# Kernel tuning notes

Measured on AMD Instinct MI355X. Metric: run time of the kernel, lower is better.

The kernel has to match this reference:

```python
import jax, jax.numpy as jnp
import numpy as np

B, T, D, N = 16, 512, 1024, 16


def setup_inputs() -> dict:
    key = jax.random.key(0)
    ks = jax.random.split(key, 6)
    x = jax.random.normal(ks[0], (B, T, D), dtype=jnp.float32)
    h_tape_init = jax.random.normal(ks[1], (B, N, D), dtype=jnp.float32) * 0.1
    h_work_init = jnp.zeros((B, D), dtype=jnp.float32)
    W_h = jax.random.normal(ks[2], (D, D), dtype=jnp.float32) * 0.02
    W_xz = jax.random.normal(ks[3], (2 * D, D), dtype=jnp.float32) * 0.02
    b_h = jnp.zeros((D,), dtype=jnp.float32)
    W_write = jax.random.normal(ks[4], (D, D), dtype=jnp.float32) * 0.02
    return {"x": x, "h_tape_init": h_tape_init, "h_work_init": h_work_init,
            "W_h": W_h, "W_xz": W_xz, "b_h": b_h, "W_write": W_write}


def _e29a_scan(x, h_tape_init, h_work_init, W_h, W_xz, b_h, W_write):
    d = W_h.shape[0]
    scale = 1.0 / (d ** 0.5)
    xz = jnp.einsum('btd,ed->bte', x, W_xz)          # [B,T,2D]
    x_proj = xz[:, :, :d]                             # [B,T,D]
    z = xz[:, :, d:]                                  # [B,T,D]

    def step(carry, inp):
        h_tape, h_work = carry                        # [B,N,D], [B,D]
        x_proj_t, z_t = inp                           # [B,D], [B,D]
        read_scores = jnp.einsum('bd,bnd->bn', h_work, h_tape) * scale
        read_attn = jax.nn.softmax(read_scores, axis=-1)
        read_val = jnp.einsum('bn,bnd->bd', read_attn, h_tape)
        h_work_new = jnp.tanh(x_proj_t + h_work @ W_h.T + read_val + b_h)
        write_val = h_work_new @ W_write.T            # [B,D]
        write_scores = jnp.einsum('bd,bnd->bn', write_val, h_tape) * scale
        write_attn = jax.nn.softmax(write_scores, axis=-1)
        wa = write_attn[:, :, None]                   # [B,N,1]
        h_tape_new = h_tape * (1.0 - wa) + write_val[:, None, :] * wa
        gate = jax.nn.silu(z_t + read_val + h_work_new)
        output = h_work_new * gate
        return (h_tape_new, h_work_new), output

    inputs = (jnp.swapaxes(x_proj, 0, 1), jnp.swapaxes(z, 0, 1))  # [T,B,D]
    (h_tape_final, _), out_t = jax.lax.scan(step, (h_tape_init, h_work_init), inputs)
    output_all = jnp.swapaxes(out_t, 0, 1)            # [B,T,D]
    return output_all, h_tape_final


def reference(x, h_tape_init, h_work_init, W_h, W_xz, b_h, W_write):
    return _e29a_scan(x, h_tape_init, h_work_init, W_h, W_xz, b_h, W_write)
```

## Files before the change

kernel.cpp:

```cpp
#include <hip/hip_runtime.h>

typedef _Float16 half8 __attribute__((ext_vector_type(8)));
typedef _Float16 half4_t __attribute__((ext_vector_type(4)));
typedef _Float16 half2_t __attribute__((ext_vector_type(2)));
typedef float f32x4 __attribute__((ext_vector_type(4)));
typedef float f32x2 __attribute__((ext_vector_type(2)));
typedef unsigned long long u64;
typedef unsigned int u32;

#define SCALE 0.03125f

#define XZ_OFF   0ULL
#define RING_OFF 33554432ULL
#define XBF_OFF  33554432ULL
#define WXZ_OFF  50331648ULL
#define WH_OFF   54525952ULL
#define WW_OFF   56623104ULL
#define VOTE_OFF 58720256ULL
#define SEN_OFF  58724352ULL

#define SLOTB 36864ULL
#define R_WVP 0
#define R_H   32768

union Pk2 { u64 u[2]; half8 h8; };
union PkW { u32 u; half2_t h; };

__device__ __forceinline__ u64 ldq(const u64* p, bool mall) {
    return mall ? __hip_atomic_load(p, __ATOMIC_RELAXED, __HIP_MEMORY_SCOPE_AGENT) : *p;
}
__device__ __forceinline__ void stq(u64* p, u64 v, bool mall) {
    if (mall) __hip_atomic_store(p, v, __ATOMIC_RELAXED, __HIP_MEMORY_SCOPE_AGENT); else *p = v;
}
__device__ __forceinline__ u32 ldw(const u32* p, bool mall) {
    return mall ? __hip_atomic_load(p, __ATOMIC_RELAXED, __HIP_MEMORY_SCOPE_AGENT) : *p;
}
__device__ __forceinline__ void stw(u32* p, u32 v, bool mall) {
    if (mall) __hip_atomic_store(p, v, __ATOMIC_RELAXED, __HIP_MEMORY_SCOPE_AGENT); else *p = v;
}
__device__ __forceinline__ u32 ldsen(u32* p) {
    return __hip_atomic_load(p, __ATOMIC_RELAXED, __HIP_MEMORY_SCOPE_AGENT);
}
__device__ __forceinline__ void stsen(u32* p, u32 v) {
    __hip_atomic_store(p, v, __ATOMIC_RELAXED, __HIP_MEMORY_SCOPE_AGENT);
}

#define FDOT(a,b,acc) acc = __builtin_amdgcn_fdot2((a),(b),(acc),false)
__device__ __forceinline__ half2_t hp2(half8 v, int i) {
    half2_t r; r[0] = v[2*i]; r[1] = v[2*i+1]; return r;
}

__global__ void cvt_kernel(const float* __restrict__ in, _Float16* __restrict__ o, int n4) {
    int i = blockIdx.x * 256 + threadIdx.x;
    if (i < n4) {
        f32x4 v = ((const f32x4*)in)[i];
        half4_t h;
        h[0] = (_Float16)v[0]; h[1] = (_Float16)v[1];
        h[2] = (_Float16)v[2]; h[3] = (_Float16)v[3];
        ((half4_t*)o)[i] = h;
    }
}

__launch_bounds__(256, 1)
__global__ void gemm_xz(const _Float16* __restrict__ A,
                        const _Float16* __restrict__ Bw,
                        _Float16* __restrict__ C) {
    __shared__ _Float16 As[128 * 40];
    __shared__ _Float16 Bs[128 * 40];
    const int tid = threadIdx.x;
    const int m0 = blockIdx.y * 128, n0 = blockIdx.x * 128;
    const int w = tid >> 6, lane = tid & 63;
    const int mw = (w >> 1) * 64, nw = (w & 1) * 64;
    const int row = lane & 15, q = lane >> 4;
    f32x4 acc[4][4];
    #pragma unroll
    for (int mt = 0; mt < 4; mt++)
        #pragma unroll
        for (int nt = 0; nt < 4; nt++)
            acc[mt][nt] = (f32x4){0.f, 0.f, 0.f, 0.f};

    for (int k0 = 0; k0 < 1024; k0 += 32) {
        __syncthreads();
        for (int cc = tid; cc < 512; cc += 256) {
            int r = cc >> 2, kc = (cc & 3) * 8;
            *(half8*)(&As[r * 40 + kc]) = *(const half8*)(&A[(size_t)(m0 + r) * 1024 + k0 + kc]);
            *(half8*)(&Bs[r * 40 + kc]) = *(const half8*)(&Bw[(size_t)(n0 + r) * 1024 + k0 + kc]);
        }
        __syncthreads();
        half8 af[4], bf[4];
        #pragma unroll
        for (int mt = 0; mt < 4; mt++) af[mt] = *(const half8*)(&As[(mw + mt * 16 + row) * 40 + q * 8]);
        #pragma unroll
        for (int nt = 0; nt < 4; nt++) bf[nt] = *(const half8*)(&Bs[(nw + nt * 16 + row) * 40 + q * 8]);
        #pragma unroll
        for (int mt = 0; mt < 4; mt++)
            #pragma unroll
            for (int nt = 0; nt < 4; nt++)
                acc[mt][nt] = __builtin_amdgcn_mfma_f32_16x16x32_f16(af[mt], bf[nt], acc[mt][nt], 0, 0, 0);
    }
    #pragma unroll
    for (int mt = 0; mt < 4; mt++)
        #pragma unroll
        for (int nt = 0; nt < 4; nt++)
            #pragma unroll
            for (int r = 0; r < 4; r++) {
                int gm = m0 + mw + mt * 16 + q * 4 + r;
                int gn = n0 + nw + nt * 16 + row;
                C[(size_t)gm * 2048 + gn] = (_Float16)acc[mt][nt][r];
            }
}

__launch_bounds__(512, 2)
__global__ void scan_kernel(const _Float16* __restrict__ xz,
                            const float* __restrict__ tape_in,
                            const float* __restrict__ h_in,
                            const float* __restrict__ bh,
                            const _Float16* __restrict__ wh,
                            const _Float16* __restrict__ ww,
                            char* ring,
                            u32* sen,
                            u32* vote,
                            float* __restrict__ out) {
    const int bx = blockIdx.x;
    const int g = (bx & 7) * 2 + ((bx >> 3) & 1);
    const int s = bx >> 4;
    const int tid = threadIdx.x;
    const int lane = tid & 63;
    const int cc = tid >> 3, q = tid & 7;
    const int nn = tid >> 5, c32 = tid & 31;

    __shared__ __align__(16) _Float16 h_prev[1024];
    __shared__ __align__(16) _Float16 h_own[64];
    __shared__ __align__(16) float rv_l[1024];
    __shared__ float p_l[512 * 17];
    __shared__ float sc_l[16];
    __shared__ float pad_l[10000];
    __shared__ int sh_same;

    { volatile float* vp = pad_l; vp[tid] = 0.f; }

    if (tid == 0) {
        u32 xcc;
        asm volatile("s_getreg_b32 %0, hwreg(HW_REG_XCC_ID)" : "=s"(xcc));
        xcc &= 7u;
        __hip_atomic_store(&vote[bx * 4], xcc + 1u, __ATOMIC_RELAXED, __HIP_MEMORY_SCOPE_AGENT);
        int same = 1; u32 ref = 0;
        for (int m = 0; m < 16; m++) {
            int mb = m * 16 + ((g & 1) << 3) + (g >> 1);
            u32 v; int spin = 0;
            while ((v = __hip_atomic_load(&vote[mb * 4], __ATOMIC_RELAXED, __HIP_MEMORY_SCOPE_AGENT)) == 0u) {
                if (++spin > 1000000) { v = 0xFFFFFFFFu; break; }
                __builtin_amdgcn_s_sleep(2);
            }
            if (m == 0) ref = v;
            if (v != ref || v == 0xFFFFFFFFu) same = 0;
        }
        sh_same = same;
    }
    __syncthreads();
    const bool mall = (sh_same == 0);
    bool dead = false;

    const int qx = q << 1;
    half8 whr[16];
    {
        const _Float16* wp = wh + (size_t)(s * 64 + cc) * 1024 + q * 128;
        #pragma unroll
        for (int jj = 0; jj < 16; jj++)
            whr[jj] = *(const half8*)(wp + (((jj ^ qx) & 15) * 8));
    }
    half8 wwr[2][8];
    {
        const _Float16* wp = ww + (size_t)(tid * 2) * 1024 + s * 64;
        #pragma unroll
        for (int jj = 0; jj < 2; jj++)
            #pragma unroll
            for (int kk = 0; kk < 8; kk++)
                wwr[jj][kk] = *(const half8*)(wp + jj * 1024 + kk * 8);
    }
    f32x2 tp[16];
    #pragma unroll
    for (int n = 0; n < 16; n++)
        tp[n] = *(const f32x2*)(&tape_in[(size_t)(g * 16 + n) * 1024 + tid * 2]);
    const float bhc = bh[s * 64 + cc];

    {
        f32x2 h2 = *(const f32x2*)(&h_in[(size_t)g * 1024 + tid * 2]);
        half2_t hh; hh[0] = (_Float16)h2[0]; hh[1] = (_Float16)h2[1];
        *(half2_t*)(&h_prev[tid * 2]) = hh;
    }
    __syncthreads();

    u32* senrow = sen + (size_t)(g * 16 + s) * 32;
    const int senb = g * 16;

    for (int t = 0; t <= 512; t++) {
        char* srd  = ring + (size_t)(g * 8 + ((t + 7) & 7)) * SLOTB;
        char* spub = ring + (size_t)(g * 8 + (t & 7)) * SLOTB;
        const bool havew = (t >= 1);
        float xp = 0.f, zz = 0.f;
        if (t < 512) {
            size_t m = (size_t)(g * 512 + t) * 2048 + s * 64 + cc;
            xp = (float)xz[m];
            zz = (float)xz[m + 1024];
        }
        f32x2 wv2 = (f32x2){0.f, 0.f};
        if (havew) {
            if (!dead && lane < 16) {
                int spin = 0;
                while (ldsen(&sen[(size_t)(senb + lane) * 32]) < (u32)t) {
                    if (++spin > 2000000) { dead = true; break; }
                    __builtin_amdgcn_s_sleep(1);
                }
            }
            asm volatile("" ::: "memory");
            if (tid < 128) {
                const u64* Hp = (const u64*)(srd + R_H);
                Pk2 u;
                u.u[0] = ldq(&Hp[tid * 2], mall);
                u.u[1] = ldq(&Hp[tid * 2 + 1], mall);
                *(half8*)(&h_prev[tid * 8]) = u.h8;
            }
            const u32* Wp = (const u32*)(srd + R_WVP);
            #pragma unroll
            for (int sl = 0; sl < 16; sl++) {
                PkW u; u.u = ldw(&Wp[sl * 512 + tid], mall);
                wv2[0] += (float)u.h[0]; wv2[1] += (float)u.h[1];
            }
            {
                float p[16];
                #pragma unroll
                for (int n = 0; n < 16; n++) {
                    f32x2 d = tp[n];
                    p[n] = wv2[0]*d[0] + wv2[1]*d[1];
                }
                #pragma unroll
                for (int n = 0; n < 16; n++) p_l[tid * 17 + n] = p[n];
            }
            __syncthreads();
            {
                float scw = 0.f;
                #pragma unroll
                for (int m2 = 0; m2 < 16; m2++) scw += p_l[(c32 + 32 * m2) * 17 + nn];
                #pragma unroll
                for (int d2 = 1; d2 < 32; d2 <<= 1) scw += __shfl_xor(scw, d2, 32);
                if (c32 == 0) sc_l[nn] = scw;
            }
            __syncthreads();
            {
                float e[16], mxw = -1e30f;
                #pragma unroll
                for (int n = 0; n < 16; n++) { e[n] = sc_l[n] * SCALE; mxw = fmaxf(mxw, e[n]); }
                float smw = 0.f;
                #pragma unroll
                for (int n = 0; n < 16; n++) { e[n] = __expf(e[n] - mxw); smw += e[n]; }
                float invw = 1.f / smw;
                #pragma unroll
                for (int n = 0; n < 16; n++) {
                    float wan = e[n] * invw;
                    f32x2 d = tp[n];
                    d[0] += wan * (wv2[0] - d[0]);
                    d[1] += wan * (wv2[1] - d[1]);
                    tp[n] = d;
                }
            }
        }
        if (t == 512) break;

        {
            half2_t hh = *(const half2_t*)(&h_prev[tid * 2]);
            float h0 = (float)hh[0], h1 = (float)hh[1];
            float p[16];
            #pragma unroll
            for (int n = 0; n < 16; n++) {
                f32x2 d = tp[n];
                p[n] = h0*d[0] + h1*d[1];
            }
            #pragma unroll
            for (int n = 0; n < 16; n++) p_l[tid * 17 + n] = p[n];
        }
        __syncthreads();
        float sc = 0.f;
        #pragma unroll
        for (int m2 = 0; m2 < 16; m2++) sc += p_l[(c32 + 32 * m2) * 17 + nn];
        #pragma unroll
        for (int d2 = 1; d2 < 32; d2 <<= 1) sc += __shfl_xor(sc, d2, 32);
        if (c32 == 0) sc_l[nn] = sc;
        __syncthreads();
        float r[16], mx = -1e30f;
        #pragma unroll
        for (int n = 0; n < 16; n++) { r[n] = sc_l[n] * SCALE; mx = fmaxf(mx, r[n]); }
        float sm = 0.f;
        #pragma unroll
        for (int n = 0; n < 16; n++) { r[n] = __expf(r[n] - mx); sm += r[n]; }
        float inv = 1.f / sm;
        f32x2 rv2 = (f32x2){0.f, 0.f};
        #pragma unroll
        for (int n = 0; n < 16; n++) {
            float ra = r[n] * inv;
            rv2[0] += ra * tp[n][0];
            rv2[1] += ra * tp[n][1];
        }
        *(f32x2*)(&rv_l[tid * 2]) = rv2;
        float a0 = 0.f, a1 = 0.f, a2 = 0.f, a3 = 0.f;
        #pragma unroll
        for (int jj = 0; jj < 16; jj++) {
            half8 hp8 = *(const half8*)(&h_prev[q * 128 + (((jj ^ qx) & 15) * 8)]);
            half8 wc = whr[jj];
            FDOT(hp2(wc,0), hp2(hp8,0), a0);
            FDOT(hp2(wc,1), hp2(hp8,1), a1);
            FDOT(hp2(wc,2), hp2(hp8,2), a2);
            FDOT(hp2(wc,3), hp2(hp8,3), a3);
        }
        float av = (a0 + a1) + (a2 + a3);
        av += __shfl_xor(av, 1);
        av += __shfl_xor(av, 2);
        av += __shfl_xor(av, 4);
        __syncthreads();
        float rd = rv_l[s * 64 + cc];
        float hv = tanhf(av + xp + rd + bhc);
        float g2 = zz + rd + hv;
        float o = hv * g2 / (1.f + __expf(-g2));
        if (q == 0) h_own[cc] = (_Float16)hv;
        __syncthreads();
        half8 hr[8];
        #pragma unroll
        for (int kk = 0; kk < 8; kk++) hr[kk] = *(const half8*)(&h_own[kk * 8]);
        float w0 = 0.f, w1 = 0.f;
        #pragma unroll
        for (int kk = 0; kk < 8; kk++) {
            half8 h8 = hr[kk];
            #pragma unroll
            for (int pp = 0; pp < 4; pp++) {
                FDOT(hp2(wwr[0][kk],pp), hp2(h8,pp), w0);
                FDOT(hp2(wwr[1][kk],pp), hp2(h8,pp), w1);
            }
        }
        {
            PkW wq;
            wq.h = (half2_t){(_Float16)w0, (_Float16)w1};
            stw(&((u32*)(spub + R_WVP))[s * 512 + tid], wq.u, mall);
            if (tid < 8) {
                Pk2 u; u.h8 = *(const half8*)(&h_own[tid * 8]);
                u64* Hp = (u64*)(spub + R_H);
                stq(&Hp[s * 16 + tid * 2],     u.u[0], mall);
                stq(&Hp[s * 16 + tid * 2 + 1], u.u[1], mall);
            }
        }
        __syncthreads();
        if (tid == 0) stsen(senrow, (u32)(t + 1));
        if (q == 0) out[(size_t)(g * 512 + t) * 1024 + s * 64 + cc] = o;
    }
    if (s == 0) {
        #pragma unroll
        for (int n = 0; n < 16; n++)
            *(f32x2*)(&out[8388608ULL + (size_t)(g * 16 + n) * 1024 + tid * 2]) = tp[n];
    }
}

extern "C" void kernel_launch(void* const* d_in, const int* in_sizes, int n_in,
                              void* d_out, int out_size, void* d_ws, size_t ws_size,
                              hipStream_t stream) {
    const float* x     = (const float*)d_in[0];
    const float* tape0 = (const float*)d_in[1];
    const float* h0    = (const float*)d_in[2];
    const float* Wh    = (const float*)d_in[3];
    const float* Wxz   = (const float*)d_in[4];
    const float* bh    = (const float*)d_in[5];
    const float* Ww    = (const float*)d_in[6];

    char* ws = (char*)d_ws;
    _Float16* xbf   = (_Float16*)(ws + XBF_OFF);
    _Float16* wxzbf = (_Float16*)(ws + WXZ_OFF);
    _Float16* whbf  = (_Float16*)(ws + WH_OFF);
    _Float16* wwbf  = (_Float16*)(ws + WW_OFF);
    _Float16* xzbf  = (_Float16*)(ws + XZ_OFF);
    char* ring      = ws + RING_OFF;
    u32* vote       = (u32*)(ws + VOTE_OFF);
    u32* sen        = (u32*)(ws + SEN_OFF);

    hipMemsetAsync(ws + VOTE_OFF, 0, 4096 + 32768, stream);

    cvt_kernel<<<8192, 256, 0, stream>>>(x, xbf, 2097152);
    cvt_kernel<<<2048, 256, 0, stream>>>(Wxz, wxzbf, 524288);
    cvt_kernel<<<1024, 256, 0, stream>>>(Wh, whbf, 262144);
    cvt_kernel<<<1024, 256, 0, stream>>>(Ww, wwbf, 262144);

    gemm_xz<<<dim3(16, 64), 256, 0, stream>>>(xbf, wxzbf, xzbf);

    scan_kernel<<<256, 512, 0, stream>>>(xzbf, tape0, h0, bh, whbf, wwbf,
                                         ring, sen, vote, (float*)d_out);
}
```

Measured before the change: 2.697 ms.

## Fuse write and read attention score reductions via algebraic tape-update identity

Computes read scores against the pre-update tape by expanding the tape update algebraically: each new score becomes (1-wa)*<h,tape> + wa*<h,write_val>. This lets the write-score and read-score reductions share one LDS staging pass and one pair of barriers, where before they needed two separate pairs. Read values are formed from the old tape plus a beta*write_val term, and the tape update is applied afterwards. The cost is extra arithmetic, a wider LDS scratch row, and slightly different floating-point rounding.

```diff
diff --git a/kernel.cpp b/kernel.cpp
--- a/kernel.cpp
+++ b/kernel.cpp
@@ -132,12 +132,12 @@
     __shared__ __align__(16) _Float16 h_prev[1024];
     __shared__ __align__(16) _Float16 h_own[64];
     __shared__ __align__(16) float rv_l[1024];
-    __shared__ float p_l[512 * 17];
-    __shared__ float sc_l[16];
-    __shared__ float pad_l[10000];
+    __shared__ float p_l[512 * 35];
+    __shared__ float sc_l[33];
+    __shared__ float pad_l[1100];
     __shared__ int sh_same;
 
-    { volatile float* vp = pad_l; vp[tid] = 0.f; }
+    if (tid < 1100) { volatile float* vp = pad_l; vp[tid] = 0.f; }
 
     if (tid == 0) {
         u32 xcc;
@@ -184,9 +184,11 @@
         tp[n] = *(const f32x2*)(&tape_in[(size_t)(g * 16 + n) * 1024 + tid * 2]);
     const float bhc = bh[s * 64 + cc];
 
+    half2_t own2;
     {
         f32x2 h2 = *(const f32x2*)(&h_in[(size_t)g * 1024 + tid * 2]);
         half2_t hh; hh[0] = (_Float16)h2[0]; hh[1] = (_Float16)h2[1];
+        own2 = hh;
         *(half2_t*)(&h_prev[tid * 2]) = hh;
     }
     __syncthreads();
@@ -214,6 +216,7 @@
                 }
             }
             asm volatile("" ::: "memory");
+            { PkW u; u.u = ldw(&((const u32*)(srd + R_H))[tid], mall); own2 = u.h; }
             if (tid < 128) {
                 const u64* Hp = (const u64*)(srd + R_H);
                 Pk2 u;
@@ -227,81 +230,121 @@
                 PkW u; u.u = ldw(&Wp[sl * 512 + tid], mall);
                 wv2[0] += (float)u.h[0]; wv2[1] += (float)u.h[1];
             }
-            {
-                float p[16];
+        }
+        {
+            float h0 = (float)own2[0], h1 = (float)own2[1];
+            if (havew) {
                 #pragma unroll
                 for (int n = 0; n < 16; n++) {
                     f32x2 d = tp[n];
-                    p[n] = wv2[0]*d[0] + wv2[1]*d[1];
+                    p_l[tid * 35 + n] = wv2[0]*d[0] + wv2[1]*d[1];
                 }
-                #pragma unroll
-                for (int n = 0; n < 16; n++) p_l[tid * 17 + n] = p[n];
-            }
-            __syncthreads();
-            {
-                float scw = 0.f;
-                #pragma unroll
-                for (int m2 = 0; m2 < 16; m2++) scw += p_l[(c32 + 32 * m2) * 17 + nn];
-                #pragma unroll
-                for (int d2 = 1; d2 < 32; d2 <<= 1) scw += __shfl_xor(scw, d2, 32);
-                if (c32 == 0) sc_l[nn] = scw;
-            }
-            __syncthreads();
-            {
-                float e[16], mxw = -1e30f;
-                #pragma unroll
-                for (int n = 0; n < 16; n++) { e[n] = sc_l[n] * SCALE; mxw = fmaxf(mxw, e[n]); }
-                float smw = 0.f;
-                #pragma unroll
-                for (int n = 0; n < 16; n++) { e[n] = __expf(e[n] - mxw); smw += e[n]; }
-                float invw = 1.f / smw;
+                if (t < 512)
+                    p_l[tid * 35 + 32] = h0*wv2[0] + h1*wv2[1];
+            }
+            if (t < 512) {
                 #pragma unroll
                 for (int n = 0; n < 16; n++) {
-                    float wan = e[n] * invw;
                     f32x2 d = tp[n];
-                    d[0] += wan * (wv2[0] - d[0]);
-                    d[1] += wan * (wv2[1] - d[1]);
-                    tp[n] = d;
+                    p_l[tid * 35 + 16 + n] = h0*d[0] + h1*d[1];
                 }
             }
         }
-        if (t == 512) break;
-
-        {
-            half2_t hh = *(const half2_t*)(&h_prev[tid * 2]);
-            float h0 = (float)hh[0], h1 = (float)hh[1];
-            float p[16];
+        __syncthreads();
+        if (havew) {
+            float sw = 0.f;
+            #pragma unroll
+            for (int m2 = 0; m2 < 16; m2++) sw += p_l[(c32 + 32 * m2) * 35 + nn];
+            #pragma unroll
+            for (int d2 = 1; d2 < 32; d2 <<= 1) sw += __shfl_xor(sw, d2, 32);
+            if (c32 == 0) sc_l[nn] = sw;
+            if (nn == 0 && t < 512) {
+                float hw = 0.f;
+                #pragma unroll
+                for (int m2 = 0; m2 < 16; m2++) hw += p_l[(c32 + 32 * m2) * 35 + 32];
+                #pragma unroll
+                for (int d2 = 1; d2 < 32; d2 <<= 1) hw += __shfl_xor(hw, d2, 32);
+                if (c32 == 0) sc_l[32] = hw;
+            }
+        }
+        if (t < 512) {
+            float sq = 0.f;
+            #pragma unroll
+            for (int m2 = 0; m2 < 16; m2++) sq += p_l[(c32 + 32 * m2) * 35 + 16 + nn];
+            #pragma unroll
+            for (int d2 = 1; d2 < 32; d2 <<= 1) sq += __shfl_xor(sq, d2, 32);
+            if (c32 == 0) sc_l[16 + nn] = sq;
+        }
+        __syncthreads();
+        float wan[16];
+        if (havew) {
+            float e[16], mxw = -1e30f;
+            #pragma unroll
+            for (int n = 0; n < 16; n++) { e[n] = sc_l[n] * SCALE; mxw = fmaxf(mxw, e[n]); }
+            float smw = 0.f;
+            #pragma unroll
+            for (int n = 0; n < 16; n++) { e[n] = __expf(e[n] - mxw); smw += e[n]; }
+            float invw = 1.f / smw;
+            #pragma unroll
+            for (int n = 0; n < 16; n++) wan[n] = e[n] * invw;
+        }
+        if (t == 512) {
             #pragma unroll
             for (int n = 0; n < 16; n++) {
                 f32x2 d = tp[n];
-                p[n] = h0*d[0] + h1*d[1];
-            }
-            #pragma unroll
-            for (int n = 0; n < 16; n++) p_l[tid * 17 + n] = p[n];
-        }
-        __syncthreads();
-        float sc = 0.f;
-        #pragma unroll
-        for (int m2 = 0; m2 < 16; m2++) sc += p_l[(c32 + 32 * m2) * 17 + nn];
-        #pragma unroll
-        for (int d2 = 1; d2 < 32; d2 <<= 1) sc += __shfl_xor(sc, d2, 32);
-        if (c32 == 0) sc_l[nn] = sc;
-        __syncthreads();
+                d[0] += wan[n] * (wv2[0] - d[0]);
+                d[1] += wan[n] * (wv2[1] - d[1]);
+                tp[n] = d;
+            }
+            break;
+        }
         float r[16], mx = -1e30f;
-        #pragma unroll
-        for (int n = 0; n < 16; n++) { r[n] = sc_l[n] * SCALE; mx = fmaxf(mx, r[n]); }
+        if (havew) {
+            float hwv = sc_l[32];
+            #pragma unroll
+            for (int n = 0; n < 16; n++) {
+                r[n] = ((1.f - wan[n]) * sc_l[16 + n] + wan[n] * hwv) * SCALE;
+                mx = fmaxf(mx, r[n]);
+            }
+        } else {
+            #pragma unroll
+            for (int n = 0; n < 16; n++) { r[n] = sc_l[16 + n] * SCALE; mx = fmaxf(mx, r[n]); }
+        }
         float sm = 0.f;
         #pragma unroll
         for (int n = 0; n < 16; n++) { r[n] = __expf(r[n] - mx); sm += r[n]; }
         float inv = 1.f / sm;
         f32x2 rv2 = (f32x2){0.f, 0.f};
-        #pragma unroll
-        for (int n = 0; n < 16; n++) {
-            float ra = r[n] * inv;
-            rv2[0] += ra * tp[n][0];
-            rv2[1] += ra * tp[n][1];
+        if (havew) {
+            float beta = 0.f;
+            #pragma unroll
+            for (int n = 0; n < 16; n++) {
+                float ran = r[n] * inv;
+                float c = ran * (1.f - wan[n]);
+                rv2[0] += c * tp[n][0];
+                rv2[1] += c * tp[n][1];
+                beta += ran * wan[n];
+            }
+            rv2[0] += beta * wv2[0];
+            rv2[1] += beta * wv2[1];
+        } else {
+            #pragma unroll
+            for (int n = 0; n < 16; n++) {
+                float ran = r[n] * inv;
+                rv2[0] += ran * tp[n][0];
+                rv2[1] += ran * tp[n][1];
+            }
         }
         *(f32x2*)(&rv_l[tid * 2]) = rv2;
+        if (havew) {
+            #pragma unroll
+            for (int n = 0; n < 16; n++) {
+                f32x2 d = tp[n];
+                d[0] += wan[n] * (wv2[0] - d[0]);
+                d[1] += wan[n] * (wv2[1] - d[1]);
+                tp[n] = d;
+            }
+        }
         float a0 = 0.f, a1 = 0.f, a2 = 0.f, a3 = 0.f;
         #pragma unroll
         for (int jj = 0; jj < 16; jj++) {
```

Result: slower. 7.095 ms (+163.1%).
